# Performance work log

Measured on AMD Instinct MI355X. Metric: run time of the kernel, lower is better.

The kernel has to match this reference:

```python
import jax, jax.numpy as jnp
import numpy as np

N, R, E, H, D_MAX = 1024, 8192, 1024, 4, 48
DH = E // H
P_EDGE = 16.0 / R  # average in-degree ~16


def setup_inputs() -> dict:
    key = jax.random.key(0)
    ks = jax.random.split(key, 6)
    s = 0.02
    return {
        "target": jax.random.normal(ks[0], (N, E), jnp.float32),
        "source": jax.random.normal(ks[1], (R, E), jnp.float32),
        "adj": (jax.random.uniform(ks[2], (N, R)) < P_EDGE).astype(jnp.float32),
        "W_trans": jax.random.normal(ks[3], (E, E), jnp.float32) * s,
        "b_trans": jnp.zeros((E,), jnp.float32),
        "in_proj_w": jax.random.normal(ks[4], (3 * E, E), jnp.float32) * s,
        "in_proj_b": jnp.zeros((3 * E,), jnp.float32),
        "out_w": jax.random.normal(ks[5], (E, E), jnp.float32) * s,
        "out_b": jnp.zeros((E,), jnp.float32),
        "unit_id": 0,
    }


def reference(target, source, adj, W_trans, b_trans, in_proj_w, in_proj_b, out_w, out_b, unit_id):
    # source = relu(trans_fc(source))
    src = jax.nn.relu(source @ W_trans.T + b_trans)  # [R, E]

    # build padded neighbor index lists (torch loops per node; here vectorized)
    deg = adj.sum(axis=1).astype(jnp.int32)                # [N]
    order = jnp.argsort(-adj, axis=1)[:, :D_MAX]           # stable: 1-columns first, ascending col idx
    valid = jnp.arange(D_MAX)[None, :] < deg[:, None]      # [N, D] True = real neighbor
    neigh = jnp.where(valid, order, 0)                     # pad with index 0 (masked, like torch)
    kv_in = src[neigh]                                     # [N, D, E] gathered neighbor feats

    # nn.MultiheadAttention: q=target (len-1 query), k=v=padded neighbors
    Wq, Wk, Wv = jnp.split(in_proj_w, 3, axis=0)
    bq, bk, bv = jnp.split(in_proj_b, 3)
    q = (target @ Wq.T + bq).reshape(-1, H, DH)            # [N, H, dh]
    k = (kv_in @ Wk.T + bk).reshape(-1, D_MAX, H, DH)      # [N, D, H, dh]
    v = (kv_in @ Wv.T + bv).reshape(-1, D_MAX, H, DH)

    scores = jnp.einsum('nhd,nkhd->nhk', q, k) / np.float32(np.sqrt(DH))  # [N, H, D]
    # key_padding_mask: padded slots -> -inf; give zero-degree nodes one dummy
    # unmasked slot so softmax stays finite (their output is zeroed below)
    safe_valid = valid.at[:, 0].set(valid[:, 0] | (deg == 0))
    scores = jnp.where(safe_valid[:, None, :], scores, -jnp.inf)
    attn = jax.nn.softmax(scores, axis=-1)
    out = jnp.einsum('nhk,nkhd->nhd', attn, v).reshape(-1, E)
    out = out @ out_w.T + out_b

    # scatter back: inactive (degree-0) nodes stay zero, like att_res_padded
    return jnp.where((deg > 0)[:, None], out, jnp.zeros((), out.dtype))
```

## Files before the change

kernel.cpp:

```cpp
#include <hip/hip_runtime.h>

#define N_NODES 1024
#define R_SRC   8192
#define E_DIM   1024
#define H_HEADS 4
#define DH_DIM  256
#define D_MAXN  48
#define NCONVB  1024

typedef __attribute__((ext_vector_type(8))) short short8;
typedef __attribute__((ext_vector_type(4))) float f32x4;

__device__ __forceinline__ unsigned short f2bf(float f) {
    unsigned u = __float_as_uint(f);
    unsigned r = u + 0x7fffu + ((u >> 16) & 1u);
    return (unsigned short)(r >> 16);
}
__device__ __forceinline__ float bf2f(unsigned short b) {
    return __uint_as_float(((unsigned)b) << 16);
}
__device__ __forceinline__ void gload16(const void* g, void* l) {
    __builtin_amdgcn_global_load_lds(
        (const __attribute__((address_space(1))) unsigned int*)g,
        (__attribute__((address_space(3))) unsigned int*)l,
        16, 0, 0);
}
template<int N> __device__ __forceinline__ void vwait() {
    if constexpr (N == 8)       asm volatile("s_waitcnt vmcnt(8)" ::: "memory");
    else if constexpr (N == 6)  asm volatile("s_waitcnt vmcnt(6)" ::: "memory");
    else if constexpr (N == 1)  asm volatile("s_waitcnt vmcnt(1)" ::: "memory");
    else                        asm volatile("s_waitcnt vmcnt(0)" ::: "memory");
}

struct GD {
    const unsigned short* A;
    const unsigned short* B;
    const float* bias;
    void* C;
    int N, K, nbx, relu, outbf;
    const int* rowmask;
};

template<int BM, int BN>
__global__ __launch_bounds__(512) void gemm_t(GD d0, GD d1, int split)
{
    constexpr int AI = BM / 64;
    constexpr int BI = BN / 64;
    constexpr int VN = AI + BI;
    constexpr int FM = BM / 32;
    constexpr int FN = BN / 64;

    __shared__ __align__(16) unsigned short lds[3][(BM + BN) * 64];

    int bid = blockIdx.x;
    const int nwg = gridDim.x;
    bid = (bid & 7) * (nwg >> 3) + (bid >> 3);

    GD d; int q;
    if (bid < split) { d = d0; q = bid; }
    else             { d = d1; q = bid - split; }
    const int m0 = (q / d.nbx) * BM;
    const int n0 = (q % d.nbx) * BN;
    const int K  = d.K;

    const int t = threadIdx.x;
    const int w = t >> 6, l = t & 63;
    const int wm = w >> 2, wn = w & 3;

    const int trow = t >> 3, tkc = t & 7;
    const int tswz = tkc ^ (trow & 7);
    const unsigned short* gA[AI];
    const unsigned short* gB[BI];
#pragma unroll
    for (int i = 0; i < AI; ++i)
        gA[i] = d.A + (size_t)(m0 + i * 64 + trow) * K + tswz * 8;
#pragma unroll
    for (int i = 0; i < BI; ++i)
        gB[i] = d.B + (size_t)(n0 + i * 64 + trow) * K + tswz * 8;

    f32x4 acc[FM][FN] = {};

    auto STAGE = [&](int c, int kt) {
        const int ko = kt * 64;
#pragma unroll
        for (int i = 0; i < AI; ++i)
            gload16(gA[i] + ko, &lds[c][(i * 512 + t) * 8]);
#pragma unroll
        for (int i = 0; i < BI; ++i)
            gload16(gB[i] + ko, &lds[c][BM * 64 + (i * 512 + t) * 8]);
    };

    const int nt = K / 64;
    STAGE(0, 0);
    STAGE(1, 1);
    vwait<VN>();
    __builtin_amdgcn_s_barrier();

    const int lr = l & 15, hi = l >> 4;
    const int rsw = l & 7;
    const int cs0 = ((0 + hi) ^ rsw) * 8;
    const int cs1 = ((4 + hi) ^ rsw) * 8;
    const int abase = (wm * (BM / 2) + lr) * 64;
    const int bbase = BM * 64 + (wn * 64 + lr) * 64;

    for (int kt = 0; kt < nt; ++kt) {
        const int cur = kt % 3;
        if (kt + 2 < nt) STAGE((kt + 2) % 3, kt + 2);

        const unsigned short* Ls = &lds[cur][0];

        short8 bv[FN][2];
#pragma unroll
        for (int fj = 0; fj < FN; ++fj) {
            bv[fj][0] = *(const short8*)&Ls[bbase + fj * 1024 + cs0];
            bv[fj][1] = *(const short8*)&Ls[bbase + fj * 1024 + cs1];
        }
#pragma unroll
        for (int g = 0; g < FM; g += 4) {
            short8 av[4][2];
#pragma unroll
            for (int fi = 0; fi < 4; ++fi) {
                av[fi][0] = *(const short8*)&Ls[abase + (g + fi) * 1024 + cs0];
                av[fi][1] = *(const short8*)&Ls[abase + (g + fi) * 1024 + cs1];
            }
            __builtin_amdgcn_s_setprio(1);
#pragma unroll
            for (int ks = 0; ks < 2; ++ks)
#pragma unroll
                for (int fi = 0; fi < 4; ++fi)
#pragma unroll
                    for (int fj = 0; fj < FN; ++fj)
                        acc[g + fi][fj] = __builtin_amdgcn_mfma_f32_16x16x32_bf16(
                            av[fi][ks], bv[fj][ks], acc[g + fi][fj], 0, 0, 0);
            __builtin_amdgcn_s_setprio(0);
        }

        asm volatile("" ::: "memory");
        __builtin_amdgcn_s_barrier();
        if (kt + 2 < nt) {
            vwait<VN>();
        } else {
            vwait<0>();
        }
        __builtin_amdgcn_s_barrier();
    }

#pragma unroll
    for (int fj = 0; fj < FN; ++fj) {
        const int c = n0 + wn * 64 + fj * 16 + lr;
        const float bvs = d.bias[c];
#pragma unroll
        for (int fi = 0; fi < FM; ++fi) {
            const int rb = m0 + wm * (BM / 2) + fi * 16 + hi * 4;
#pragma unroll
            for (int qq = 0; qq < 4; ++qq) {
                const int r = rb + qq;
                float x = acc[fi][fj][qq] + bvs;
                if (d.relu) x = fmaxf(x, 0.0f);
                if (d.rowmask && d.rowmask[r] == 0) x = 0.0f;
                if (d.outbf) ((unsigned short*)d.C)[(size_t)r * d.N + c] = f2bf(x);
                else         ((float*)d.C)[(size_t)r * d.N + c] = x;
            }
        }
    }
}

struct GS {
    const unsigned short* A;
    const unsigned short* B;
    const float* bias;
    void* C;
    int lda, ldb, ldc, K, relu, outbf;
    long long azs, bzs, czs;
    int bias_zs;
    const int* rowmask;
};

__global__ __launch_bounds__(256) void gemm_s(GS g)
{
    const int z = blockIdx.z;
    const unsigned short* A = g.A + (size_t)((long long)z * g.azs);
    const unsigned short* B = g.B + (size_t)((long long)z * g.bzs);
    const float* bias = g.bias ? g.bias + (size_t)z * g.bias_zs : nullptr;

    __shared__ __align__(16) unsigned short S[128 * 32];

    const int t = threadIdx.x;
    const int m0 = blockIdx.y * 64;
    const int n0 = blockIdx.x * 64;
    const int w = t >> 6, l = t & 63;
    const int wrow = (w >> 1) * 32;
    const int wcol = (w & 1) * 32;
    const int lr = l & 15;
    const int kg = (l >> 4) * 8;

    f32x4 acc[2][2] = {};

    const unsigned short* gp[2];
    unsigned short* lp[2];
    {
        const int c0 = t;
        gp[0] = A + (size_t)(m0 + (c0 >> 2)) * g.lda + (c0 & 3) * 8;
        lp[0] = &S[c0 * 8];
        const int c1 = t;
        gp[1] = B + (size_t)(n0 + (c1 >> 2)) * g.ldb + (c1 & 3) * 8;
        lp[1] = &S[2048 + c1 * 8];
    }

    for (int k0 = 0; k0 < g.K; k0 += 32) {
        gload16(gp[0] + k0, lp[0]);
        gload16(gp[1] + k0, lp[1]);
        __syncthreads();

        short8 af[2], bw[2];
#pragma unroll
        for (int i = 0; i < 2; ++i)
            af[i] = *(const short8*)&S[(wrow + i * 16 + lr) * 32 + kg];
#pragma unroll
        for (int j = 0; j < 2; ++j)
            bw[j] = *(const short8*)&S[2048 + (wcol + j * 16 + lr) * 32 + kg];
#pragma unroll
        for (int i = 0; i < 2; ++i)
#pragma unroll
            for (int j = 0; j < 2; ++j)
                acc[i][j] = __builtin_amdgcn_mfma_f32_16x16x32_bf16(
                    af[i], bw[j], acc[i][j], 0, 0, 0);
        __syncthreads();
    }

#pragma unroll
    for (int j = 0; j < 2; ++j) {
        const int c = n0 + wcol + j * 16 + lr;
        const float bv = bias ? bias[c] : 0.0f;
#pragma unroll
        for (int i = 0; i < 2; ++i) {
            const int rbase = m0 + wrow + i * 16 + (l >> 4) * 4;
#pragma unroll
            for (int qq = 0; qq < 4; ++qq) {
                const int r = rbase + qq;
                float x = acc[i][j][qq] + bv;
                if (g.relu) x = fmaxf(x, 0.0f);
                if (g.rowmask && g.rowmask[r] == 0) x = 0.0f;
                if (g.outbf)
                    ((unsigned short*)g.C)[(size_t)((long long)z * g.czs) + (size_t)r * g.ldc + c] = f2bf(x);
                else
                    ((float*)g.C)[(size_t)((long long)z * g.czs) + (size_t)r * g.ldc + c] = x;
            }
        }
    }
}

struct ConvArgs {
    const float* s[4];
    unsigned short* d[4];
    unsigned off[5];
};

__global__ __launch_bounds__(256) void pre_kernel(
    const float* __restrict__ adj, int* __restrict__ neigh, int* __restrict__ deg,
    ConvArgs a, const float* __restrict__ inw_f, const float* __restrict__ tgt_f,
    const float* __restrict__ in_b, unsigned short* __restrict__ WkT,
    unsigned short* __restrict__ Q_bf)
{
    __shared__ __align__(16) unsigned char smem[64 * 65 * 4];
    const int t = threadIdx.x;

    if (blockIdx.x < 256) {
        unsigned short (*QS)[64 * 32] = (unsigned short (*)[64 * 32])smem;
        const int qb = blockIdx.x;
        const int m0 = (qb >> 4) * 64;
        const int n0 = (qb & 15) * 64;
        const int w = t >> 6, l = t & 63;
        const int wrow = (w >> 1) * 32;
        const int wcol = (w & 1) * 32;
        const int lr = l & 15;
        const int kg = (l >> 4) * 8;
        const int row = t >> 2, k8 = (t & 3) * 8;

        const float* ga = tgt_f + (size_t)(m0 + row) * E_DIM + k8;
        const float* gb = inw_f + (size_t)(n0 + row) * E_DIM + k8;

        f32x4 acc[2][2] = {};

        for (int k0 = 0; k0 < E_DIM; k0 += 32) {
            float4 a0 = *(const float4*)(ga + k0);
            float4 a1 = *(const float4*)(ga + k0 + 4);
            float4 b0 = *(const float4*)(gb + k0);
            float4 b1 = *(const float4*)(gb + k0 + 4);
            short8 av, bv;
            av[0] = (short)f2bf(a0.x); av[1] = (short)f2bf(a0.y);
            av[2] = (short)f2bf(a0.z); av[3] = (short)f2bf(a0.w);
            av[4] = (short)f2bf(a1.x); av[5] = (short)f2bf(a1.y);
            av[6] = (short)f2bf(a1.z); av[7] = (short)f2bf(a1.w);
            bv[0] = (short)f2bf(b0.x); bv[1] = (short)f2bf(b0.y);
            bv[2] = (short)f2bf(b0.z); bv[3] = (short)f2bf(b0.w);
            bv[4] = (short)f2bf(b1.x); bv[5] = (short)f2bf(b1.y);
            bv[6] = (short)f2bf(b1.z); bv[7] = (short)f2bf(b1.w);
            *(short8*)&QS[0][row * 32 + k8] = av;
            *(short8*)&QS[1][row * 32 + k8] = bv;
            __syncthreads();

            short8 af[2], bw[2];
#pragma unroll
            for (int i = 0; i < 2; ++i)
                af[i] = *(const short8*)&QS[0][(wrow + i * 16 + lr) * 32 + kg];
#pragma unroll
            for (int j = 0; j < 2; ++j)
                bw[j] = *(const short8*)&QS[1][(wcol + j * 16 + lr) * 32 + kg];
#pragma unroll
            for (int i = 0; i < 2; ++i)
#pragma unroll
                for (int j = 0; j < 2; ++j)
                    acc[i][j] = __builtin_amdgcn_mfma_f32_16x16x32_bf16(
                        af[i], bw[j], acc[i][j], 0, 0, 0);
            __syncthreads();
        }

#pragma unroll
        for (int j = 0; j < 2; ++j) {
            const int c = n0 + wcol + j * 16 + lr;
            const float bv = in_b[c];
#pragma unroll
            for (int i = 0; i < 2; ++i) {
                const int rbase = m0 + wrow + i * 16 + (l >> 4) * 4;
#pragma unroll
                for (int qq = 0; qq < 4; ++qq)
                    Q_bf[(size_t)(rbase + qq) * E_DIM + c] = f2bf(acc[i][j][qq] + bv);
            }
        }
        return;
    }

    if (blockIdx.x < 512) {
        float (*tile)[65] = (float (*)[65])smem;
        const int tb = blockIdx.x - 256;
        const int h = tb >> 6, rem = tb & 63;
        const int e0 = (rem >> 2) * 64, d0 = (rem & 3) * 64;
        const int r = t >> 2, c4 = (t & 3) * 16;
        const float* tsrc = inw_f + (size_t)(E_DIM + h * 256 + d0 + r) * E_DIM + e0 + c4;
#pragma unroll
        for (int jj = 0; jj < 4; ++jj) {
            float4 v = ((const float4*)tsrc)[jj];
            tile[r][c4 + jj * 4 + 0] = v.x;
            tile[r][c4 + jj * 4 + 1] = v.y;
            tile[r][c4 + jj * 4 + 2] = v.z;
            tile[r][c4 + jj * 4 + 3] = v.w;
        }
        __syncthreads();
        const int er = t >> 2, dc = (t & 3) * 16;
        unsigned short* wout = WkT + ((size_t)h * E_DIM + e0 + er) * 256 + d0 + dc;
#pragma unroll
        for (int jj = 0; jj < 4; ++jj) {
            ushort4 o;
            o.x = f2bf(tile[dc + jj * 4 + 0][er]);
            o.y = f2bf(tile[dc + jj * 4 + 1][er]);
            o.z = f2bf(tile[dc + jj * 4 + 2][er]);
            o.w = f2bf(tile[dc + jj * 4 + 3][er]);
            ((ushort4*)wout)[jj] = o;
        }
        return;
    }

    if (blockIdx.x < (unsigned)(512 + N_NODES)) {
        int* s_cnt = (int*)smem;
        int (*s_idx)[D_MAXN] = (int (*)[D_MAXN])(smem + 16);

        const int n    = blockIdx.x - 512;
        const int w    = t >> 6;
        const int lane = t & 63;
        const float* row = adj + (size_t)n * R_SRC;

        const int seg0 = w * (R_SRC / 4);
        const unsigned long long lower = (1ULL << lane) - 1ULL;
        int total = 0;

        for (int base = seg0; base < seg0 + R_SRC / 4; base += 256) {
            const float v0 = row[base + lane];
            const float v1 = row[base + 64 + lane];
            const float v2 = row[base + 128 + lane];
            const float v3 = row[base + 192 + lane];
            const unsigned long long m0 = __ballot(v0 != 0.0f);
            const unsigned long long m1 = __ballot(v1 != 0.0f);
            const unsigned long long m2 = __ballot(v2 != 0.0f);
            const unsigned long long m3 = __ballot(v3 != 0.0f);
            int p;
            p = total + __popcll(m0 & lower);
            if (v0 != 0.0f && p < D_MAXN) s_idx[w][p] = base + lane;
            total += __popcll(m0);
            p = total + __popcll(m1 & lower);
            if (v1 != 0.0f && p < D_MAXN) s_idx[w][p] = base + 64 + lane;
            total += __popcll(m1);
            p = total + __popcll(m2 & lower);
            if (v2 != 0.0f && p < D_MAXN) s_idx[w][p] = base + 128 + lane;
            total += __popcll(m2);
            p = total + __popcll(m3 & lower);
            if (v3 != 0.0f && p < D_MAXN) s_idx[w][p] = base + 192 + lane;
            total += __popcll(m3);
        }
        if (lane == 0) s_cnt[w] = total;
        __syncthreads();

        int start = 0;
#pragma unroll
        for (int i = 0; i < 4; ++i) if (i < w) start += s_cnt[i];
        const int degree = s_cnt[0] + s_cnt[1] + s_cnt[2] + s_cnt[3];
        const int nstore = total < D_MAXN ? total : D_MAXN;
        if (lane < nstore) {
            const int gpos = start + lane;
            if (gpos < D_MAXN) neigh[n * D_MAXN + gpos] = s_idx[w][lane];
        }
        if (t == 0) deg[n] = degree;
        return;
    }

    {
        const unsigned total = a.off[4];
        const unsigned stride = NCONVB * 1024;
        for (unsigned bs = (blockIdx.x - 512 - N_NODES) * 1024; bs < total; bs += stride) {
            float4 v[4];
            unsigned idx[4];
            int ok[4];
#pragma unroll
            for (int j = 0; j < 4; ++j) {
                idx[j] = bs + j * 256 + t;
                ok[j] = idx[j] < total;
            }
            int seg[4];
#pragma unroll
            for (int j = 0; j < 4; ++j) {
                seg[j] = 0;
#pragma unroll
                for (int s = 1; s < 4; ++s) seg[j] += (idx[j] >= a.off[s]);
            }
#pragma unroll
            for (int j = 0; j < 4; ++j)
                if (ok[j]) v[j] = ((const float4*)a.s[seg[j]])[idx[j] - a.off[seg[j]]];
#pragma unroll
            for (int j = 0; j < 4; ++j) {
                if (ok[j]) {
                    ushort4 o;
                    o.x = f2bf(v[j].x); o.y = f2bf(v[j].y);
                    o.z = f2bf(v[j].z); o.w = f2bf(v[j].w);
                    ((ushort4*)a.d[seg[j]])[idx[j] - a.off[seg[j]]] = o;
                }
            }
        }
    }
}

__global__ __launch_bounds__(256) void gather_ctx(
    const float* __restrict__ Ahat, const unsigned short* __restrict__ srcrel,
    const int* __restrict__ neigh, const int* __restrict__ deg,
    unsigned short* __restrict__ ctx)
{
    const int n = blockIdx.x;
    const int t = threadIdx.x;
    const int h = t >> 6;
    const int lane = t & 63;

    unsigned short* crow = ctx + ((size_t)n * H_HEADS + h) * E_DIM + lane * 16;
    const int degree = deg[n];
    if (degree == 0) {
        ushort4 z4 = {0, 0, 0, 0};
#pragma unroll
        for (int j = 0; j < 4; ++j) ((ushort4*)crow)[j] = z4;
        return;
    }
    const int dv = degree < D_MAXN ? degree : D_MAXN;

    __shared__ int s_neigh[D_MAXN];
    if (t < dv) s_neigh[t] = neigh[n * D_MAXN + t];
    __syncthreads();

    float a[16];
    {
        const float4* ap = (const float4*)(Ahat + (size_t)n * (H_HEADS * E_DIM) + h * E_DIM + lane * 16);
#pragma unroll
        for (int j = 0; j < 4; ++j) {
            float4 v = ap[j];
            a[j * 4 + 0] = v.x; a[j * 4 + 1] = v.y; a[j * 4 + 2] = v.z; a[j * 4 + 3] = v.w;
        }
    }

    float m = -3.4e38f, sum = 0.0f;
    float cacc[16];
#pragma unroll
    for (int i = 0; i < 16; ++i) cacc[i] = 0.0f;

    const float scale = 0.0625f;

    int d = 0;
    for (; d + 1 < dv; d += 2) {
        const ushort4* rp0 = (const ushort4*)(srcrel + (size_t)s_neigh[d]     * E_DIM + lane * 16);
        const ushort4* rp1 = (const ushort4*)(srcrel + (size_t)s_neigh[d + 1] * E_DIM + lane * 16);
        ushort4 w00 = rp0[0], w01 = rp0[1], w02 = rp0[2], w03 = rp0[3];
        ushort4 w10 = rp1[0], w11 = rp1[1], w12 = rp1[2], w13 = rp1[3];
        float e0[16], e1[16];
        e0[0]=bf2f(w00.x); e0[1]=bf2f(w00.y); e0[2]=bf2f(w00.z); e0[3]=bf2f(w00.w);
        e0[4]=bf2f(w01.x); e0[5]=bf2f(w01.y); e0[6]=bf2f(w01.z); e0[7]=bf2f(w01.w);
        e0[8]=bf2f(w02.x); e0[9]=bf2f(w02.y); e0[10]=bf2f(w02.z); e0[11]=bf2f(w02.w);
        e0[12]=bf2f(w03.x); e0[13]=bf2f(w03.y); e0[14]=bf2f(w03.z); e0[15]=bf2f(w03.w);
        e1[0]=bf2f(w10.x); e1[1]=bf2f(w10.y); e1[2]=bf2f(w10.z); e1[3]=bf2f(w10.w);
        e1[4]=bf2f(w11.x); e1[5]=bf2f(w11.y); e1[6]=bf2f(w11.z); e1[7]=bf2f(w11.w);
        e1[8]=bf2f(w12.x); e1[9]=bf2f(w12.y); e1[10]=bf2f(w12.z); e1[11]=bf2f(w12.w);
        e1[12]=bf2f(w13.x); e1[13]=bf2f(w13.y); e1[14]=bf2f(w13.z); e1[15]=bf2f(w13.w);

        float s0 = 0.0f, s1 = 0.0f;
#pragma unroll
        for (int i = 0; i < 16; ++i) { s0 = fmaf(a[i], e0[i], s0); s1 = fmaf(a[i], e1[i], s1); }
#pragma unroll
        for (int off = 32; off > 0; off >>= 1) {
            s0 += __shfl_xor(s0, off);
            s1 += __shfl_xor(s1, off);
        }
        s0 *= scale; s1 *= scale;

        if (s0 > m) {
            const float f = __expf(m - s0);
            sum *= f;
#pragma unroll
            for (int i = 0; i < 16; ++i) cacc[i] *= f;
            m = s0;
        }
        {
            const float wgt = __expf(s0 - m);
            sum += wgt;
#pragma unroll
            for (int i = 0; i < 16; ++i) cacc[i] = fmaf(wgt, e0[i], cacc[i]);
        }
        if (s1 > m) {
            const float f = __expf(m - s1);
            sum *= f;
#pragma unroll
            for (int i = 0; i < 16; ++i) cacc[i] *= f;
            m = s1;
        }
        {
            const float wgt = __expf(s1 - m);
            sum += wgt;
#pragma unroll
            for (int i = 0; i < 16; ++i) cacc[i] = fmaf(wgt, e1[i], cacc[i]);
        }
    }
    for (; d < dv; ++d) {
        const ushort4* rp = (const ushort4*)(srcrel + (size_t)s_neigh[d] * E_DIM + lane * 16);
        float e[16];
#pragma unroll
        for (int j = 0; j < 4; ++j) {
            ushort4 v = rp[j];
            e[j * 4 + 0] = bf2f(v.x); e[j * 4 + 1] = bf2f(v.y);
            e[j * 4 + 2] = bf2f(v.z); e[j * 4 + 3] = bf2f(v.w);
        }
        float s = 0.0f;
#pragma unroll
        for (int i = 0; i < 16; ++i) s = fmaf(a[i], e[i], s);
#pragma unroll
        for (int off = 32; off > 0; off >>= 1) s += __shfl_xor(s, off);
        s *= scale;
        if (s > m) {
            const float f = __expf(m - s);
            sum *= f;
#pragma unroll
            for (int i = 0; i < 16; ++i) cacc[i] *= f;
            m = s;
        }
        const float wgt = __expf(s - m);
        sum += wgt;
#pragma unroll
        for (int i = 0; i < 16; ++i) cacc[i] = fmaf(wgt, e[i], cacc[i]);
    }

    const float inv = 1.0f / sum;
#pragma unroll
    for (int j = 0; j < 4; ++j) {
        ushort4 o;
        o.x = f2bf(cacc[j * 4 + 0] * inv);
        o.y = f2bf(cacc[j * 4 + 1] * inv);
        o.z = f2bf(cacc[j * 4 + 2] * inv);
        o.w = f2bf(cacc[j * 4 + 3] * inv);
        ((ushort4*)crow)[j] = o;
    }
}

extern "C" void kernel_launch(void* const* d_in, const int* in_sizes, int n_in,
                              void* d_out, int out_size, void* d_ws, size_t ws_size,
                              hipStream_t stream)
{
    const float* target  = (const float*)d_in[0];
    const float* source  = (const float*)d_in[1];
    const float* adj     = (const float*)d_in[2];
    const float* W_trans = (const float*)d_in[3];
    const float* b_trans = (const float*)d_in[4];
    const float* in_w    = (const float*)d_in[5];
    const float* in_b    = (const float*)d_in[6];
    const float* out_w   = (const float*)d_in[7];
    const float* out_b   = (const float*)d_in[8];
    float* out = (float*)d_out;

    char* ws = (char*)d_ws;
    unsigned short* src_bf    = (unsigned short*)ws; ws += (size_t)R_SRC * E_DIM * 2;
    unsigned short* wt_bf     = (unsigned short*)ws; ws += (size_t)E_DIM * E_DIM * 2;
    unsigned short* wv_bf     = (unsigned short*)ws; ws += (size_t)E_DIM * E_DIM * 2;
    unsigned short* outw_bf   = (unsigned short*)ws; ws += (size_t)E_DIM * E_DIM * 2;
    unsigned short* srcrel_bf = (unsigned short*)ws; ws += (size_t)R_SRC * E_DIM * 2;
    unsigned short* WkT_bf    = (unsigned short*)ws; ws += (size_t)H_HEADS * E_DIM * DH_DIM * 2;
    unsigned short* Q_bf      = (unsigned short*)ws; ws += (size_t)N_NODES * E_DIM * 2;
    float*          Ahat      = (float*)ws;         ws += (size_t)N_NODES * H_HEADS * E_DIM * 4;
    unsigned short* ctx_bf    = (unsigned short*)ws; ws += (size_t)N_NODES * H_HEADS * E_DIM * 2;
    unsigned short* attn_bf   = (unsigned short*)ws; ws += (size_t)N_NODES * E_DIM * 2;
    int*            neigh     = (int*)ws;            ws += (size_t)N_NODES * D_MAXN * 4;
    int*            deg       = (int*)ws;            ws += (size_t)N_NODES * 4;

    const size_t EE = (size_t)E_DIM * E_DIM;

    {
        ConvArgs a;
        const unsigned sz4[4] = {
            (unsigned)((size_t)R_SRC * E_DIM / 4),
            (unsigned)(EE / 4),
            (unsigned)(EE / 4),
            (unsigned)(EE / 4)};
        a.s[0] = source;        a.d[0] = src_bf;
        a.s[1] = W_trans;       a.d[1] = wt_bf;
        a.s[2] = in_w + 2 * EE; a.d[2] = wv_bf;
        a.s[3] = out_w;         a.d[3] = outw_bf;
        a.off[0] = 0;
        for (int i = 0; i < 4; ++i) a.off[i + 1] = a.off[i] + sz4[i];
        pre_kernel<<<512 + N_NODES + NCONVB, 256, 0, stream>>>(
            adj, neigh, deg, a, in_w, target, in_b, WkT_bf, Q_bf);
    }

    {
        GD ds;
        ds.A = src_bf; ds.B = wt_bf; ds.bias = b_trans; ds.C = srcrel_bf;
        ds.N = E_DIM; ds.K = E_DIM; ds.nbx = E_DIM / 256; ds.relu = 1; ds.outbf = 1;
        ds.rowmask = nullptr;
        const int sblocks = (R_SRC / 128) * (E_DIM / 256);
        gemm_t<128, 256><<<sblocks, 512, 0, stream>>>(ds, ds, sblocks);
    }

    {
        GS g;
        g.A = Q_bf; g.B = WkT_bf; g.bias = nullptr; g.C = Ahat;
        g.lda = E_DIM; g.ldb = DH_DIM; g.ldc = H_HEADS * E_DIM; g.K = DH_DIM;
        g.relu = 0; g.outbf = 0;
        g.azs = DH_DIM;
        g.bzs = (long long)E_DIM * DH_DIM;
        g.czs = E_DIM;
        g.bias_zs = 0; g.rowmask = nullptr;
        gemm_s<<<dim3(E_DIM / 64, N_NODES / 64, H_HEADS), 256, 0, stream>>>(g);
    }

    gather_ctx<<<N_NODES, 256, 0, stream>>>(Ahat, srcrel_bf, neigh, deg, ctx_bf);

    {
        GS g;
        g.A = ctx_bf; g.B = wv_bf; g.bias = in_b + 2 * E_DIM; g.C = attn_bf;
        g.lda = H_HEADS * E_DIM; g.ldb = E_DIM; g.ldc = E_DIM; g.K = E_DIM;
        g.relu = 0; g.outbf = 1;
        g.azs = E_DIM;
        g.bzs = (long long)DH_DIM * E_DIM;
        g.czs = DH_DIM;
        g.bias_zs = DH_DIM; g.rowmask = nullptr;
        gemm_s<<<dim3(DH_DIM / 64, N_NODES / 64, H_HEADS), 256, 0, stream>>>(g);
    }

    {
        GS g;
        g.A = attn_bf; g.B = outw_bf; g.bias = out_b; g.C = out;
        g.lda = E_DIM; g.ldb = E_DIM; g.ldc = E_DIM; g.K = E_DIM;
        g.relu = 0; g.outbf = 0; g.azs = 0; g.bzs = 0; g.czs = 0; g.bias_zs = 0;
        g.rowmask = deg;
        gemm_s<<<dim3(E_DIM / 64, N_NODES / 64, 1), 256, 0, stream>>>(g);
    }
}
```

Before: 113.8 us.

## Double-buffer Q-projection tiles via async global-to-LDS loads with swizzled fp32 staging

The Q-projection block of pre_kernel now stages fp32 tiles of target and Wq straight into LDS with global_load_lds, double-buffered, prefetching two k-steps ahead. Previously each step loaded through registers, converted, stored and synchronised. Conversion to bf16 now happens after the LDS read, and an XOR swizzle is meant to avoid bank conflicts. This hides global latency at the cost of twice the LDS footprint (fp32 staging, 32KB) and repeated conversions per wave.

```diff
diff --git a/kernel.cpp b/kernel.cpp
--- a/kernel.cpp
+++ b/kernel.cpp
@@ -28,6 +28,7 @@
 template<int N> __device__ __forceinline__ void vwait() {
     if constexpr (N == 8)       asm volatile("s_waitcnt vmcnt(8)" ::: "memory");
     else if constexpr (N == 6)  asm volatile("s_waitcnt vmcnt(6)" ::: "memory");
+    else if constexpr (N == 4)  asm volatile("s_waitcnt vmcnt(4)" ::: "memory");
     else if constexpr (N == 1)  asm volatile("s_waitcnt vmcnt(1)" ::: "memory");
     else                        asm volatile("s_waitcnt vmcnt(0)" ::: "memory");
 }
@@ -262,11 +263,11 @@
     const float* __restrict__ in_b, unsigned short* __restrict__ WkT,
     unsigned short* __restrict__ Q_bf)
 {
-    __shared__ __align__(16) unsigned char smem[64 * 65 * 4];
+    __shared__ __align__(16) unsigned char smem[32768];
     const int t = threadIdx.x;
 
     if (blockIdx.x < 256) {
-        unsigned short (*QS)[64 * 32] = (unsigned short (*)[64 * 32])smem;
+        float* QS = (float*)smem;
         const int qb = blockIdx.x;
         const int m0 = (qb >> 4) * 64;
         const int n0 = (qb & 15) * 64;
@@ -274,46 +275,72 @@
         const int wrow = (w >> 1) * 32;
         const int wcol = (w & 1) * 32;
         const int lr = l & 15;
-        const int kg = (l >> 4) * 8;
-        const int row = t >> 2, k8 = (t & 3) * 8;
-
-        const float* ga = tgt_f + (size_t)(m0 + row) * E_DIM + k8;
-        const float* gb = inw_f + (size_t)(n0 + row) * E_DIM + k8;
+        const int hi = l >> 4;
+        const int rsw = lr & 7;
+
+        const int srow = t >> 3, sc = t & 7;
+        const int sswz = (sc ^ (srow & 7)) * 4;
+        const float* gqa = tgt_f + (size_t)(m0 + srow) * E_DIM + sswz;
+        const float* gqb = inw_f + (size_t)(n0 + srow) * E_DIM + sswz;
+
+        auto QSTAGE = [&](int b, int k0) {
+            float* base = QS + b * 4096;
+            gload16(gqa + k0,                 base + t * 4);
+            gload16(gqa + k0 + 32 * E_DIM,    base + (t + 256) * 4);
+            gload16(gqb + k0,                 base + 2048 + t * 4);
+            gload16(gqb + k0 + 32 * E_DIM,    base + 2048 + (t + 256) * 4);
+        };
 
         f32x4 acc[2][2] = {};
 
-        for (int k0 = 0; k0 < E_DIM; k0 += 32) {
-            float4 a0 = *(const float4*)(ga + k0);
-            float4 a1 = *(const float4*)(ga + k0 + 4);
-            float4 b0 = *(const float4*)(gb + k0);
-            float4 b1 = *(const float4*)(gb + k0 + 4);
-            short8 av, bv;
-            av[0] = (short)f2bf(a0.x); av[1] = (short)f2bf(a0.y);
-            av[2] = (short)f2bf(a0.z); av[3] = (short)f2bf(a0.w);
-            av[4] = (short)f2bf(a1.x); av[5] = (short)f2bf(a1.y);
-            av[6] = (short)f2bf(a1.z); av[7] = (short)f2bf(a1.w);
-            bv[0] = (short)f2bf(b0.x); bv[1] = (short)f2bf(b0.y);
-            bv[2] = (short)f2bf(b0.z); bv[3] = (short)f2bf(b0.w);
-            bv[4] = (short)f2bf(b1.x); bv[5] = (short)f2bf(b1.y);
-            bv[6] = (short)f2bf(b1.z); bv[7] = (short)f2bf(b1.w);
-            *(short8*)&QS[0][row * 32 + k8] = av;
-            *(short8*)&QS[1][row * 32 + k8] = bv;
-            __syncthreads();
+        QSTAGE(0, 0);
+        QSTAGE(1, 32);
+        vwait<4>();
+        __builtin_amdgcn_s_barrier();
+
+        const int ca = ((2 * hi + 0) ^ rsw) * 4;
+        const int cb = ((2 * hi + 1) ^ rsw) * 4;
+
+        for (int kt = 0; kt < 32; ++kt) {
+            const float* base = QS + (kt & 1) * 4096;
 
             short8 af[2], bw[2];
 #pragma unroll
-            for (int i = 0; i < 2; ++i)
-                af[i] = *(const short8*)&QS[0][(wrow + i * 16 + lr) * 32 + kg];
-#pragma unroll
-            for (int j = 0; j < 2; ++j)
-                bw[j] = *(const short8*)&QS[1][(wcol + j * 16 + lr) * 32 + kg];
+            for (int i = 0; i < 2; ++i) {
+                const int rr = wrow + i * 16 + lr;
+                float4 f0 = *(const float4*)&base[rr * 32 + ca];
+                float4 f1 = *(const float4*)&base[rr * 32 + cb];
+                af[i][0] = (short)f2bf(f0.x); af[i][1] = (short)f2bf(f0.y);
+                af[i][2] = (short)f2bf(f0.z); af[i][3] = (short)f2bf(f0.w);
+                af[i][4] = (short)f2bf(f1.x); af[i][5] = (short)f2bf(f1.y);
+                af[i][6] = (short)f2bf(f1.z); af[i][7] = (short)f2bf(f1.w);
+            }
+#pragma unroll
+            for (int j = 0; j < 2; ++j) {
+                const int rr = wcol + j * 16 + lr;
+                float4 f0 = *(const float4*)&base[2048 + rr * 32 + ca];
+                float4 f1 = *(const float4*)&base[2048 + rr * 32 + cb];
+                bw[j][0] = (short)f2bf(f0.x); bw[j][1] = (short)f2bf(f0.y);
+                bw[j][2] = (short)f2bf(f0.z); bw[j][3] = (short)f2bf(f0.w);
+                bw[j][4] = (short)f2bf(f1.x); bw[j][5] = (short)f2bf(f1.y);
+                bw[j][6] = (short)f2bf(f1.z); bw[j][7] = (short)f2bf(f1.w);
+            }
 #pragma unroll
             for (int i = 0; i < 2; ++i)
 #pragma unroll
                 for (int j = 0; j < 2; ++j)
                     acc[i][j] = __builtin_amdgcn_mfma_f32_16x16x32_bf16(
                         af[i], bw[j], acc[i][j], 0, 0, 0);
-            __syncthreads();
+
+            asm volatile("" ::: "memory");
+            __builtin_amdgcn_s_barrier();
+            if (kt + 2 < 32) {
+                QSTAGE(kt & 1, (kt + 2) * 32);
+                vwait<4>();
+            } else {
+                vwait<0>();
+            }
+            __builtin_amdgcn_s_barrier();
         }
 
 #pragma unroll
```

Result: no change. 115.4 us (+1.5%).

## Triple-buffer LDS staging in gemm_s to overlap global loads with MFMA

Applied to the files above, without the earlier changes.

Converts the small-tile gemm_s kernel from a single LDS buffer with load-then-sync per k-step into a 3-stage ring buffer. Tiles for k+2 are prefetched via global_load_lds while the current tile is consumed, with vmcnt waits and raw s_barrier replacing __syncthreads. The goal is to hide global memory latency behind MFMA work, at the cost of three times the LDS and an extra barrier per iteration. It also swaps the vmcnt(1) helper for vmcnt(4)/(2) variants.

```diff
diff --git a/kernel.cpp b/kernel.cpp
--- a/kernel.cpp
+++ b/kernel.cpp
@@ -28,7 +28,8 @@
 template<int N> __device__ __forceinline__ void vwait() {
     if constexpr (N == 8)       asm volatile("s_waitcnt vmcnt(8)" ::: "memory");
     else if constexpr (N == 6)  asm volatile("s_waitcnt vmcnt(6)" ::: "memory");
-    else if constexpr (N == 1)  asm volatile("s_waitcnt vmcnt(1)" ::: "memory");
+    else if constexpr (N == 4)  asm volatile("s_waitcnt vmcnt(4)" ::: "memory");
+    else if constexpr (N == 2)  asm volatile("s_waitcnt vmcnt(2)" ::: "memory");
     else                        asm volatile("s_waitcnt vmcnt(0)" ::: "memory");
 }
 
@@ -183,7 +184,7 @@
     const unsigned short* B = g.B + (size_t)((long long)z * g.bzs);
     const float* bias = g.bias ? g.bias + (size_t)z * g.bias_zs : nullptr;
 
-    __shared__ __align__(16) unsigned short S[128 * 32];
+    __shared__ __align__(16) unsigned short S[3][128 * 32];
 
     const int t = threadIdx.x;
     const int m0 = blockIdx.y * 64;
@@ -196,36 +197,48 @@
 
     f32x4 acc[2][2] = {};
 
-    const unsigned short* gp[2];
-    unsigned short* lp[2];
-    {
-        const int c0 = t;
-        gp[0] = A + (size_t)(m0 + (c0 >> 2)) * g.lda + (c0 & 3) * 8;
-        lp[0] = &S[c0 * 8];
-        const int c1 = t;
-        gp[1] = B + (size_t)(n0 + (c1 >> 2)) * g.ldb + (c1 & 3) * 8;
-        lp[1] = &S[2048 + c1 * 8];
-    }
-
-    for (int k0 = 0; k0 < g.K; k0 += 32) {
-        gload16(gp[0] + k0, lp[0]);
-        gload16(gp[1] + k0, lp[1]);
-        __syncthreads();
+    const unsigned short* gp0 = A + (size_t)(m0 + (t >> 2)) * g.lda + (t & 3) * 8;
+    const unsigned short* gp1 = B + (size_t)(n0 + (t >> 2)) * g.ldb + (t & 3) * 8;
+
+    auto STAGE = [&](int c, int k0) {
+        gload16(gp0 + k0, &S[c][t * 8]);
+        gload16(gp1 + k0, &S[c][2048 + t * 8]);
+    };
+
+    const int nt = g.K / 32;
+    STAGE(0, 0);
+    STAGE(1, 32);
+    vwait<2>();
+    __builtin_amdgcn_s_barrier();
+
+    for (int kt = 0; kt < nt; ++kt) {
+        const int cur = kt % 3;
+        if (kt + 2 < nt) STAGE((kt + 2) % 3, (kt + 2) * 32);
+
+        const unsigned short* Ls = &S[cur][0];
 
         short8 af[2], bw[2];
 #pragma unroll
         for (int i = 0; i < 2; ++i)
-            af[i] = *(const short8*)&S[(wrow + i * 16 + lr) * 32 + kg];
+            af[i] = *(const short8*)&Ls[(wrow + i * 16 + lr) * 32 + kg];
 #pragma unroll
         for (int j = 0; j < 2; ++j)
-            bw[j] = *(const short8*)&S[2048 + (wcol + j * 16 + lr) * 32 + kg];
+            bw[j] = *(const short8*)&Ls[2048 + (wcol + j * 16 + lr) * 32 + kg];
 #pragma unroll
         for (int i = 0; i < 2; ++i)
 #pragma unroll
             for (int j = 0; j < 2; ++j)
                 acc[i][j] = __builtin_amdgcn_mfma_f32_16x16x32_bf16(
                     af[i], bw[j], acc[i][j], 0, 0, 0);
-        __syncthreads();
+
+        asm volatile("" ::: "memory");
+        __builtin_amdgcn_s_barrier();
+        if (kt + 2 < nt) {
+            vwait<2>();
+        } else {
+            vwait<0>();
+        }
+        __builtin_amdgcn_s_barrier();
     }
 
 #pragma unroll
```

Result: faster. 105.9 us, median of 2 (-6.9%).
